# Kernel tuning notes

Measured on AMD Instinct MI355X. Metric: run time of the kernel, lower is better.

The kernel has to match this reference:

```python
import jax, jax.numpy as jnp
import numpy as np


def _forward(x, target, c0, Wm0, bm0, Wm1, bm1, Wf10, bf10, Wf11, bf11,
             Wf20, bf20, Wf21, bf21, Wh0, bh0, Wh1, bh1):
    dt = x.dtype
    F = jnp.array([[1., 0., 1., 0.], [0., 1., 0., 1.], [0., 0., 1., 0.], [0., 0., 0., 1.]], dtype=dt)
    Hm = jnp.array([[1., 0., 0., 0.], [0., 1., 0., 0.]], dtype=dt)
    G = jnp.array([[0.5, 0.], [0., 0.5], [1., 0.], [0., 1.]], dtype=dt)
    Q = 0.01 * jnp.eye(4, dtype=dt)
    R = jnp.eye(2, dtype=dt)
    B = x.shape[0]
    s0 = target[:, 0, :]                                   # [B,4] init state from label
    P0 = jnp.broadcast_to(jnp.eye(4, dtype=dt), (B, 4, 4))

    def step(carry, meas):                                  # meas: [B,2]
        c, s, P = carry                                     # [B,h],[B,4],[B,4,4]
        sn = s / 60.0
        # MUG: memory update gate
        cu = jnp.tanh(jnp.concatenate([c, sn], -1) @ Wm0 + bm0)
        cs = jnp.concatenate([cu, sn], -1)
        # SPG: state prediction gate
        d = jnp.tanh(cs @ Wf10 + bf10) @ Wf11 + bf11        # [B,2]
        s_pred = s @ F.T + d @ G.T                          # [B,4]
        pv = jnp.tanh(cs @ Wf20 + bf20) @ Wf21 + bf21       # [B,4]
        P_pred = jnp.einsum('ij,bjk,lk->bil', F, P, F) + pv[:, :, None] * pv[:, None, :] + Q
        # SUG: state update gate
        inna = meas - s_pred @ Hm.T                         # [B,2]
        hv = jnp.tanh(jnp.concatenate([cu, sn, meas / 60.0], -1) @ Wh0 + bh0) @ Wh1 + bh1
        S = jnp.einsum('ij,bjk,lk->bil', Hm, P_pred, Hm) + hv[:, :, None] * hv[:, None, :] + R
        PHt = jnp.einsum('bij,kj->bik', P_pred, Hm)         # [B,4,2]
        K = PHt @ jnp.linalg.inv(S)                         # [B,4,2]
        s_upd = s_pred + jnp.einsum('bij,bj->bi', K, inna)
        P_upd = P_pred - K @ S @ jnp.swapaxes(K, 1, 2)
        c_new = jnp.tanh(jnp.concatenate([cu, meas / 60.0, s_upd / 60.0], -1) @ Wm1 + bm1)
        return (c_new, s_upd, P_upd), s_upd

    _, outs = jax.lax.scan(step, (c0, s0, P0), jnp.swapaxes(x, 0, 1))
    return jnp.swapaxes(outs, 0, 1)                         # [B,T,4]


def setup_inputs() -> dict:
    key = jax.random.key(0)
    B, T, H, SD, MD = 2048, 128, 256, 4, 2
    ks = jax.random.split(key, 12)

    def lin(k, fin, fout):
        kw, kb = jax.random.split(k)
        sc = 1.0 / np.sqrt(fin)
        return (jax.random.uniform(kw, (fin, fout), jnp.float32, -sc, sc),
                jax.random.uniform(kb, (fout,), jnp.float32, -sc, sc))

    Wm0, bm0 = lin(ks[0], SD + H, H)
    Wm1, bm1 = lin(ks[1], SD + H + MD, H)
    Wf10, bf10 = lin(ks[2], SD + H, H)
    Wf11, bf11 = lin(ks[3], H, 2)
    Wf20, bf20 = lin(ks[4], SD + H, H)
    Wf21, bf21 = lin(ks[5], H, SD)
    Wh0, bh0 = lin(ks[6], SD + H + MD, H)
    Wh1, bh1 = lin(ks[7], H, MD)
    x = jax.random.normal(ks[8], (B, T, MD), jnp.float32) * 60.0
    target = jax.random.normal(ks[9], (B, T, SD), jnp.float32) * 60.0
    c0 = jax.random.uniform(ks[10], (B, H), jnp.float32, -0.1, 0.1)
    return dict(x=x, target=target, c0=c0, Wm0=Wm0, bm0=bm0, Wm1=Wm1, bm1=bm1,
                Wf10=Wf10, bf10=bf10, Wf11=Wf11, bf11=bf11, Wf20=Wf20, bf20=bf20,
                Wf21=Wf21, bf21=bf21, Wh0=Wh0, bh0=bh0, Wh1=Wh1, bh1=bh1)


def reference(x, target, c0, Wm0, bm0, Wm1, bm1, Wf10, bf10, Wf11, bf11,
              Wf20, bf20, Wf21, bf21, Wh0, bh0, Wh1, bh1):
    return _forward(x, target, c0, Wm0, bm0, Wm1, bm1, Wf10, bf10, Wf11, bf11,
                    Wf20, bf20, Wf21, bf21, Wh0, bh0, Wh1, bh1)
```

## Files before the change

kernel.cpp:

```cpp
#include <hip/hip_runtime.h>

typedef unsigned short u16;
typedef unsigned char  u8;
typedef signed char    s8;
typedef __bf16 bf16x8 __attribute__((ext_vector_type(8)));
typedef int    i32x4  __attribute__((ext_vector_type(4)));

#define T_STEPS 128
#define S2STR   776


__device__ __forceinline__ float bf2f(u16 h) {
  union { unsigned int u; float f; } v; v.u = ((unsigned int)h) << 16; return v.f;
}
__device__ __forceinline__ u16 f2bf(float f) {
  union { float f; unsigned int u; } v; v.f = f;
  unsigned int u = v.u;
  return (u16)((u + 0x7fffu + ((u >> 16) & 1u)) >> 16);
}
__device__ __forceinline__ unsigned int pack2(float a, float b) {
  return (unsigned int)f2bf(a) | ((unsigned int)f2bf(b) << 16);
}
__device__ __forceinline__ float clampf(float x, float lo, float hi) {
  return fmaxf(lo, fminf(x, hi));
}
__device__ __forceinline__ float tanh_fast(float x) {
  float e = __expf(2.0f * x);
  return 1.0f - 2.0f * __builtin_amdgcn_rcpf(e + 1.0f);
}
__device__ __forceinline__ int q8(float v, float s) {
  int q = __float2int_rn(v * s);
  return max(-127, min(127, q));
}
__device__ __forceinline__ unsigned int pack4q(float a, float b, float c, float d, float s) {
  return (unsigned int)(q8(a,s) & 255) | ((unsigned int)(q8(b,s) & 255) << 8) |
         ((unsigned int)(q8(c,s) & 255) << 16) | ((unsigned int)(q8(d,s) & 255) << 24);
}
__device__ __forceinline__ s8 qw(float w) {
  int q = __float2int_rn(w * 2032.0f);
  return (s8)max(-127, min(127, q));
}

__device__ __forceinline__ i32x4 mfma_i8(i32x4 a, i32x4 b, i32x4 acc) {
  asm volatile("v_mfma_i32_16x16x64_i8 %0, %1, %2, %0" : "+v"(acc) : "v"(a), "v"(b));
  return acc;
}
__device__ __forceinline__ i32x4 accfence(i32x4 acc) {
  asm volatile("s_nop 7\n\ts_nop 7" : "+v"(acc));
  return acc;
}

__global__ void egbrnn_prep(
    const float* __restrict__ Wm0, const float* __restrict__ Wm1,
    const float* __restrict__ Wf10, const float* __restrict__ Wf11,
    const float* __restrict__ Wf20, const float* __restrict__ Wf21,
    const float* __restrict__ Wh0, const float* __restrict__ Wh1,
    const float* __restrict__ bm0, const float* __restrict__ bm1,
    const float* __restrict__ bf10, const float* __restrict__ bf11,
    const float* __restrict__ bf20, const float* __restrict__ bf21,
    const float* __restrict__ bh0, const float* __restrict__ bh1,
    u8* __restrict__ ws)
{
  int idx = blockIdx.x * 256 + threadIdx.x;
  if (idx < 81920) {
    int tile = idx >> 10, r = idx & 1023;
    int lane = r >> 4, j = r & 15;
    int ft = tile / 5, kt = tile % 5;
    int m = (ft << 4) + (lane & 15);
    int k = kt * 64 + ((lane >> 4) << 4) + j;
    float w = (k < 260) ? Wm0[k * 256 + m] : 0.f;
    ((s8*)ws)[idx] = qw(w);
    return;
  }
  idx -= 81920;
  if (idx < 245760) {
    int tile = idx >> 10, r = idx & 1023;
    int lane = r >> 4, j = r & 15;
    int ft = tile / 5, kt = tile % 5;
    int F = (ft << 4) + (lane & 15);
    int k = kt * 64 + ((lane >> 4) << 4) + j;
    int sel = F >> 8, col = F & 255;
    float w = 0.f;
    if (sel == 0)      { if (k < 260) w = Wf10[k * 256 + col]; }
    else if (sel == 1) { if (k < 260) w = Wf20[k * 256 + col]; }
    else               { if (k < 262) w = Wh0 [k * 256 + col]; }
    ((s8*)ws)[81920 + idx] = qw(w);
    return;
  }
  idx -= 245760;
  if (idx < 81920) {
    int tile = idx >> 10, r = idx & 1023;
    int lane = r >> 4, j = r & 15;
    int ft = tile / 5, kt = tile % 5;
    int m = (ft << 4) + (lane & 15);
    int row = -1;
    if (kt < 4) row = kt * 64 + ((lane >> 4) << 4) + j;
    else {
      int kk = ((lane >> 4) << 4) + j;
      if (kk < 2) row = 256 + kk;
      else if (kk < 6) row = 258 + (kk - 2);
    }
    float w = (row >= 0) ? Wm1[row * 256 + m] : 0.f;
    ((s8*)ws)[327680 + idx] = qw(w);
    return;
  }
  idx -= 81920;
  if (idx < 1288) {
    float* BIAS = (float*)(ws + 409600);
    float h;
    if (idx < 256) h = bm0[idx];
    else if (idx < 1024) {
      int f = idx - 256;
      h = (f < 256) ? bf10[f] : (f < 512 ? bf20[f - 256] : bh0[f - 512]);
    } else if (idx < 1280) h = bm1[idx - 1024];
    else {
      int i2 = idx - 1280;
      h = (i2 < 2) ? bf11[i2] : (i2 < 6 ? bf21[i2 - 2] : bh1[i2 - 6]);
    }
    BIAS[idx] = h;
    return;
  }
  idx -= 1288;
  if (idx < 2048) {
    int o = idx >> 8, k = idx & 255;
    float v;
    if (o < 2)      v = Wf11[k * 2 + o];
    else if (o < 6) v = Wf21[k * 4 + (o - 2)];
    else            v = Wh1[k * 2 + (o - 6)];
    ((u16*)(ws + 414752))[idx] = f2bf(v);
  }
}

__global__ __launch_bounds__(1024, 4) void egbrnn_main(
    const float* __restrict__ x, const float* __restrict__ target,
    const float* __restrict__ c0, const u8* __restrict__ wsp,
    float* __restrict__ out)
{
  __shared__ __align__(16) u8  ACT1[5 * 1024];
  __shared__ __align__(16) u8  ACT2[6 * 1024];
  __shared__ __align__(16) u16 S2O[16 * S2STR];
  __shared__ __align__(16) u16 HWs[2048];
  __shared__ __align__(16) float SM[128];

  const float* BIAS = (const float*)(wsp + 409600);
  const float* B1 = BIAS;
  const float* B2 = BIAS + 256;
  const float* B3 = BIAS + 1024;
  const float* BS = BIAS + 1280;

  const float SA = 0.0625f / 16129.0f;
  const float SB = 0.5f / 16129.0f;
  const float SC_SN = 127.0f / 480.0f;

  const int tid = threadIdx.x;
  const int wave = tid >> 6;
  const int lane = tid & 63;
  const int nidx = lane & 15;
  const int q = lane >> 4;
  const int boff = (q << 8) + (nidx << 4);
  const int loff = lane << 4;
  const int b0 = blockIdx.x << 4;

  const int wvu = __builtin_amdgcn_readfirstlane(wave);
  const u8* pk1w  = wsp + wvu * 5120;
  const u8* pk2w0 = wsp + 81920 + wvu * 5120;
  const u8* pk2w1 = wsp + 81920 + (wvu + 16) * 5120;
  const u8* pk2w2 = wsp + 81920 + (wvu + 32) * 5120;
  const u8* pk3w  = wsp + 327680 + wvu * 5120;

  for (int i = tid; i < 2048; i += 1024) HWs[i] = ((const u16*)(wsp + 414752))[i];

  {
    int p = tid << 2;
    int tile = p >> 10, r = p & 1023;
    int b = (r >> 4) & 15;
    int kg = tile * 64 + ((r >> 8) << 4) + (r & 15);
    float4 cv = *(const float4*)(c0 + (((size_t)(b0 + b)) << 8) + kg);
    *(unsigned int*)(ACT1 + p) = pack4q(cv.x, cv.y, cv.z, cv.w, 127.0f);
  }

  float s0v = 0.f, s1v = 0.f, s2v = 0.f, s3v = 0.f;
  float P[16];
#pragma unroll
  for (int i = 0; i < 16; ++i) P[i] = 0.f;
  if (tid < 16) {
    float4 tg = *(const float4*)(target + (((size_t)(b0 + tid)) << 9));
    s0v = tg.x; s1v = tg.y; s2v = tg.z; s3v = tg.w;
    P[0] = P[5] = P[10] = P[15] = 1.f;
    unsigned int snp = pack4q(s0v, s1v, s2v, s3v, SC_SN);
    *(unsigned int*)(ACT1 + 4096 + (tid << 4)) = snp;
    *(unsigned int*)(ACT2 + 4096 + (tid << 4)) = snp;
  }
  __syncthreads();

  const int hpair = tid >> 2, hpart = tid & 3;
  const int hb = hpair & 15, ho = hpair >> 4;
  const int hcolBase = (ho < 2) ? 0 : ((ho < 6) ? 256 : 512);

  const i32x4 zero4 = {0, 0, 0, 0};

  for (int t = 0; t < T_STEPS; ++t) {
    if (tid < 16) {
      float2 mm = *(const float2*)(x + (((size_t)(b0 + tid)) << 8) + (t << 1));
      int qm0 = q8(mm.x, SC_SN), qm1 = q8(mm.y, SC_SN);
      *(u16*)(ACT2 + 4096 + (tid << 4) + 4) = (u16)((qm0 & 255) | ((qm1 & 255) << 8));
    }
    {
      i32x4 aA = zero4, aB = zero4;
#pragma unroll
      for (int kt = 0; kt < 4; ++kt) {
        i32x4 bfr = *(const i32x4*)(ACT1 + (kt << 10) + boff);
        i32x4 af  = *(const i32x4*)(pk1w + (kt << 10) + loff);
        aA = mfma_i8(af, bfr, aA);
      }
      {
        i32x4 bfr = *(const i32x4*)(ACT1 + 4096 + boff);
        i32x4 af  = *(const i32x4*)(pk1w + 4096 + loff);
        aB = mfma_i8(af, bfr, aB);
      }
      aA = accfence(aA); aB = accfence(aB);
      const int f0 = (wave << 4) + (q << 2);
      const float4 bs = *(const float4*)(B1 + f0);
      float v0 = tanh_fast(clampf((float)aA[0] * SA + (float)aB[0] * SB + bs.x, -30.f, 30.f));
      float v1 = tanh_fast(clampf((float)aA[1] * SA + (float)aB[1] * SB + bs.y, -30.f, 30.f));
      float v2 = tanh_fast(clampf((float)aA[2] * SA + (float)aB[2] * SB + bs.z, -30.f, 30.f));
      float v3 = tanh_fast(clampf((float)aA[3] * SA + (float)aB[3] * SB + bs.w, -30.f, 30.f));
      const int kk = f0 & 63;
      *(unsigned int*)(ACT2 + ((f0 >> 6) << 10) + (((f0 >> 4) & 3) << 8) + (nidx << 4) + (kk & 15)) =
          pack4q(v0, v1, v2, v3, 127.0f);
    }
    __syncthreads();
    {
      i32x4 cA[3], cB[3];
#pragma unroll
      for (int i = 0; i < 3; ++i) { cA[i] = zero4; cB[i] = zero4; }
#pragma unroll
      for (int kt = 0; kt < 5; ++kt) {
        i32x4 bfr = *(const i32x4*)(ACT2 + (kt << 10) + boff);
        i32x4 af0 = *(const i32x4*)(pk2w0 + (kt << 10) + loff);
        i32x4 af1 = *(const i32x4*)(pk2w1 + (kt << 10) + loff);
        i32x4 af2 = *(const i32x4*)(pk2w2 + (kt << 10) + loff);
        if (kt < 4) {
          cA[0] = mfma_i8(af0, bfr, cA[0]);
          cA[1] = mfma_i8(af1, bfr, cA[1]);
          cA[2] = mfma_i8(af2, bfr, cA[2]);
        } else {
          cB[0] = mfma_i8(af0, bfr, cB[0]);
          cB[1] = mfma_i8(af1, bfr, cB[1]);
          cB[2] = mfma_i8(af2, bfr, cB[2]);
        }
      }
#pragma unroll
      for (int i = 0; i < 3; ++i) {
        cA[i] = accfence(cA[i]); cB[i] = accfence(cB[i]);
        const int ft = wave + 16 * i;
        const int f0 = (ft << 4) + (q << 2);
        const float4 bs = *(const float4*)(B2 + f0);
        float v0 = tanh_fast(clampf((float)cA[i][0] * SA + (float)cB[i][0] * SB + bs.x, -30.f, 30.f));
        float v1 = tanh_fast(clampf((float)cA[i][1] * SA + (float)cB[i][1] * SB + bs.y, -30.f, 30.f));
        float v2 = tanh_fast(clampf((float)cA[i][2] * SA + (float)cB[i][2] * SB + bs.z, -30.f, 30.f));
        float v3 = tanh_fast(clampf((float)cA[i][3] * SA + (float)cB[i][3] * SB + bs.w, -30.f, 30.f));
        uint2 pv; pv.x = pack2(v0, v1); pv.y = pack2(v2, v3);
        *(uint2*)(S2O + nidx * S2STR + f0) = pv;
      }
    }
    __syncthreads();
    if (tid < 512) {
      const u16* ap = S2O + hb * S2STR + hcolBase + (hpart << 6);
      const u16* wp = HWs + (ho << 8) + (hpart << 6);
      float p = 0.f;
#pragma unroll
      for (int i = 0; i < 8; ++i) {
        bf16x8 av = *(const bf16x8*)(ap + (i << 3));
        bf16x8 wv = *(const bf16x8*)(wp + (i << 3));
#pragma unroll
        for (int j = 0; j < 8; ++j) p += (float)av[j] * (float)wv[j];
      }
      p += __shfl_xor(p, 1);
      p += __shfl_xor(p, 2);
      if (hpart == 0) SM[hb * 8 + ho] = clampf(p + BS[ho], -64.f, 64.f);
    }
    __syncthreads();
    if (tid < 16) {
      const float* sm = SM + tid * 8;
      float d0 = sm[0], d1 = sm[1];
      float pv[4] = { sm[2], sm[3], sm[4], sm[5] };
      float hv0 = sm[6], hv1 = sm[7];
      float2 mm = *(const float2*)(x + (((size_t)(b0 + tid)) << 8) + (t << 1));
      float m0 = mm.x, m1 = mm.y;
      float sp[4];
      sp[0] = s0v + s2v + 0.5f * d0;
      sp[1] = s1v + s3v + 0.5f * d1;
      sp[2] = s2v + d0;
      sp[3] = s3v + d1;
      float FP[16], Pp[16];
#pragma unroll
      for (int j = 0; j < 4; ++j) {
        FP[0 * 4 + j] = P[0 * 4 + j] + P[2 * 4 + j];
        FP[1 * 4 + j] = P[1 * 4 + j] + P[3 * 4 + j];
        FP[2 * 4 + j] = P[2 * 4 + j];
        FP[3 * 4 + j] = P[3 * 4 + j];
      }
#pragma unroll
      for (int i = 0; i < 4; ++i) {
        Pp[i * 4 + 0] = FP[i * 4 + 0] + FP[i * 4 + 2];
        Pp[i * 4 + 1] = FP[i * 4 + 1] + FP[i * 4 + 3];
        Pp[i * 4 + 2] = FP[i * 4 + 2];
        Pp[i * 4 + 3] = FP[i * 4 + 3];
      }
#pragma unroll
      for (int i = 0; i < 4; ++i)
#pragma unroll
        for (int j = 0; j < 4; ++j) Pp[i * 4 + j] += pv[i] * pv[j];
#pragma unroll
      for (int i = 0; i < 4; ++i) Pp[i * 4 + i] += 0.01f;
      float in0 = m0 - sp[0], in1 = m1 - sp[1];
      float S00 = Pp[0] + hv0 * hv0 + 1.0f;
      float S01 = Pp[1] + hv0 * hv1;
      float S10 = Pp[4] + hv1 * hv0;
      float S11 = Pp[5] + hv1 * hv1 + 1.0f;
      float det = S00 * S11 - S01 * S10;
      if (!(fabsf(det) > 1e-8f)) det = 1e-8f;
      float idet = 1.0f / det;
      float i00 =  S11 * idet, i01 = -S01 * idet, i10 = -S10 * idet, i11 = S00 * idet;
      float K[8], KS[8], su[4];
#pragma unroll
      for (int i = 0; i < 4; ++i) {
        K[i * 2 + 0] = Pp[i * 4 + 0] * i00 + Pp[i * 4 + 1] * i10;
        K[i * 2 + 1] = Pp[i * 4 + 0] * i01 + Pp[i * 4 + 1] * i11;
      }
#pragma unroll
      for (int i = 0; i < 4; ++i)
        su[i] = clampf(sp[i] + K[i * 2 + 0] * in0 + K[i * 2 + 1] * in1, -131072.f, 131072.f);
#pragma unroll
      for (int i = 0; i < 4; ++i) {
        KS[i * 2 + 0] = K[i * 2 + 0] * S00 + K[i * 2 + 1] * S10;
        KS[i * 2 + 1] = K[i * 2 + 0] * S01 + K[i * 2 + 1] * S11;
      }
#pragma unroll
      for (int i = 0; i < 4; ++i)
#pragma unroll
        for (int j = 0; j < 4; ++j)
          P[i * 4 + j] = clampf(
              Pp[i * 4 + j] - (KS[i * 2 + 0] * K[j * 2 + 0] + KS[i * 2 + 1] * K[j * 2 + 1]),
              -131072.f, 131072.f);
      s0v = su[0]; s1v = su[1]; s2v = su[2]; s3v = su[3];
      float4 ov; ov.x = su[0]; ov.y = su[1]; ov.z = su[2]; ov.w = su[3];
      *(float4*)(out + (((size_t)(b0 + tid)) << 9) + (t << 2)) = ov;
      unsigned int snp = pack4q(su[0], su[1], su[2], su[3], SC_SN);
      *(unsigned int*)(ACT1 + 4096 + (tid << 4)) = snp;
      *(unsigned int*)(ACT2 + 4096 + (tid << 4)) = snp;
      int qm0 = q8(m0, SC_SN), qm1 = q8(m1, SC_SN);
      *(unsigned int*)(ACT2 + 5120 + (tid << 4)) =
          (unsigned int)(qm0 & 255) | ((unsigned int)(qm1 & 255) << 8) |
          ((snp & 255) << 16) | (((snp >> 8) & 255) << 24);
      *(u16*)(ACT2 + 5120 + (tid << 4) + 4) = (u16)((snp >> 16) & 0xffffu);
    }
    __syncthreads();
    {
      i32x4 aA = zero4, aB = zero4;
#pragma unroll
      for (int kt = 0; kt < 4; ++kt) {
        i32x4 bfr = *(const i32x4*)(ACT2 + (kt << 10) + boff);
        i32x4 af  = *(const i32x4*)(pk3w + (kt << 10) + loff);
        aA = mfma_i8(af, bfr, aA);
      }
      {
        i32x4 bfr = *(const i32x4*)(ACT2 + 5120 + boff);
        i32x4 af  = *(const i32x4*)(pk3w + 4096 + loff);
        aB = mfma_i8(af, bfr, aB);
      }
      aA = accfence(aA); aB = accfence(aB);
      const int f0 = (wave << 4) + (q << 2);
      const float4 bs = *(const float4*)(B3 + f0);
      float v0 = tanh_fast(clampf((float)aA[0] * SA + (float)aB[0] * SB + bs.x, -30.f, 30.f));
      float v1 = tanh_fast(clampf((float)aA[1] * SA + (float)aB[1] * SB + bs.y, -30.f, 30.f));
      float v2 = tanh_fast(clampf((float)aA[2] * SA + (float)aB[2] * SB + bs.z, -30.f, 30.f));
      float v3 = tanh_fast(clampf((float)aA[3] * SA + (float)aB[3] * SB + bs.w, -30.f, 30.f));
      const int kk = f0 & 63;
      *(unsigned int*)(ACT1 + ((f0 >> 6) << 10) + (((f0 >> 4) & 3) << 8) + (nidx << 4) + (kk & 15)) =
          pack4q(v0, v1, v2, v3, 127.0f);
    }
    __syncthreads();
  }
}

extern "C" void kernel_launch(void* const* d_in, const int* in_sizes, int n_in,
                              void* d_out, int out_size, void* d_ws, size_t ws_size,
                              hipStream_t stream) {
  const float* x    = (const float*)d_in[0];
  const float* tgt  = (const float*)d_in[1];
  const float* c0   = (const float*)d_in[2];
  const float* Wm0  = (const float*)d_in[3];
  const float* bm0  = (const float*)d_in[4];
  const float* Wm1  = (const float*)d_in[5];
  const float* bm1  = (const float*)d_in[6];
  const float* Wf10 = (const float*)d_in[7];
  const float* bf10 = (const float*)d_in[8];
  const float* Wf11 = (const float*)d_in[9];
  const float* bf11 = (const float*)d_in[10];
  const float* Wf20 = (const float*)d_in[11];
  const float* bf20 = (const float*)d_in[12];
  const float* Wf21 = (const float*)d_in[13];
  const float* bf21 = (const float*)d_in[14];
  const float* Wh0  = (const float*)d_in[15];
  const float* bh0  = (const float*)d_in[16];
  const float* Wh1  = (const float*)d_in[17];
  const float* bh1  = (const float*)d_in[18];
  u8* ws     = (u8*)d_ws;
  float* out = (float*)d_out;

  egbrnn_prep<<<dim3(1614), dim3(256), 0, stream>>>(
      Wm0, Wm1, Wf10, Wf11, Wf20, Wf21, Wh0, Wh1,
      bm0, bm1, bf10, bf11, bf20, bf21, bh0, bh1, ws);
  egbrnn_main<<<dim3(128), dim3(1024), 0, stream>>>(x, tgt, c0, ws, out);
}
```

Before: 928.8 us.

## Stage first gate weights in LDS and pad head-stage smem rows to avoid bank conflicts

The packed int8 weights for the first memory-update GEMM (80 KB) are copied into shared memory once per block, so each timestep reads them from LDS rather than global/L2. The bf16 S2O activations and head weights are re-laid out with a 16-byte pad every 64 elements to reduce LDS bank conflicts in the small head dot products. The extra 80 KB of LDS per block can lower occupancy (the launch bounds ask for 4 blocks) and adds a one-time copy cost.

```diff
diff --git a/kernel.cpp b/kernel.cpp
--- a/kernel.cpp
+++ b/kernel.cpp
@@ -7,7 +7,8 @@
 typedef int    i32x4  __attribute__((ext_vector_type(4)));
 
 #define T_STEPS 128
-#define S2STR   776
+#define S2ROW 1744
+#define HWROW 560
 
 
 __device__ __forceinline__ float bf2f(u16 h) {
@@ -136,10 +137,11 @@
     const float* __restrict__ c0, const u8* __restrict__ wsp,
     float* __restrict__ out)
 {
-  __shared__ __align__(16) u8  ACT1[5 * 1024];
-  __shared__ __align__(16) u8  ACT2[6 * 1024];
-  __shared__ __align__(16) u16 S2O[16 * S2STR];
-  __shared__ __align__(16) u16 HWs[2048];
+  __shared__ __align__(16) u8 LPK1[81920];
+  __shared__ __align__(16) u8 ACT1[5 * 1024];
+  __shared__ __align__(16) u8 ACT2[6 * 1024];
+  __shared__ __align__(16) u8 S2O[16 * S2ROW];
+  __shared__ __align__(16) u8 HWs[8 * HWROW];
   __shared__ __align__(16) float SM[128];
 
   const float* BIAS = (const float*)(wsp + 409600);
@@ -162,13 +164,19 @@
   const int b0 = blockIdx.x << 4;
 
   const int wvu = __builtin_amdgcn_readfirstlane(wave);
-  const u8* pk1w  = wsp + wvu * 5120;
   const u8* pk2w0 = wsp + 81920 + wvu * 5120;
   const u8* pk2w1 = wsp + 81920 + (wvu + 16) * 5120;
   const u8* pk2w2 = wsp + 81920 + (wvu + 32) * 5120;
   const u8* pk3w  = wsp + 327680 + wvu * 5120;
-
-  for (int i = tid; i < 2048; i += 1024) HWs[i] = ((const u16*)(wsp + 414752))[i];
+  const u8* lpk1w = LPK1 + wvu * 5120;
+
+  for (int i = tid; i < 5120; i += 1024)
+    *(i32x4*)(LPK1 + (i << 4)) = *(const i32x4*)(wsp + (i << 4));
+
+  for (int i = tid; i < 2048; i += 1024) {
+    int o = i >> 8, k = i & 255;
+    *(u16*)(HWs + o * HWROW + (k << 1) + ((k >> 6) << 4)) = ((const u16*)(wsp + 414752))[i];
+  }
 
   {
     int p = tid << 2;
@@ -196,6 +204,9 @@
   const int hpair = tid >> 2, hpart = tid & 3;
   const int hb = hpair & 15, ho = hpair >> 4;
   const int hcolBase = (ho < 2) ? 0 : ((ho < 6) ? 256 : 512);
+  const int hf = hcolBase + (hpart << 6);
+  const int hapOff = hb * S2ROW + (hf << 1) + ((hf >> 6) << 4);
+  const int hwpOff = ho * HWROW + hpart * 144;
 
   const i32x4 zero4 = {0, 0, 0, 0};
 
@@ -210,12 +221,12 @@
 #pragma unroll
       for (int kt = 0; kt < 4; ++kt) {
         i32x4 bfr = *(const i32x4*)(ACT1 + (kt << 10) + boff);
-        i32x4 af  = *(const i32x4*)(pk1w + (kt << 10) + loff);
+        i32x4 af  = *(const i32x4*)(lpk1w + (kt << 10) + loff);
         aA = mfma_i8(af, bfr, aA);
       }
       {
         i32x4 bfr = *(const i32x4*)(ACT1 + 4096 + boff);
-        i32x4 af  = *(const i32x4*)(pk1w + 4096 + loff);
+        i32x4 af  = *(const i32x4*)(lpk1w + 4096 + loff);
         aB = mfma_i8(af, bfr, aB);
       }
       aA = accfence(aA); aB = accfence(aB);
@@ -225,8 +236,7 @@
       float v1 = tanh_fast(clampf((float)aA[1] * SA + (float)aB[1] * SB + bs.y, -30.f, 30.f));
       float v2 = tanh_fast(clampf((float)aA[2] * SA + (float)aB[2] * SB + bs.z, -30.f, 30.f));
       float v3 = tanh_fast(clampf((float)aA[3] * SA + (float)aB[3] * SB + bs.w, -30.f, 30.f));
-      const int kk = f0 & 63;
-      *(unsigned int*)(ACT2 + ((f0 >> 6) << 10) + (((f0 >> 4) & 3) << 8) + (nidx << 4) + (kk & 15)) =
+      *(unsigned int*)(ACT2 + ((f0 >> 6) << 10) + (((f0 >> 4) & 3) << 8) + (nidx << 4) + (f0 & 15)) =
           pack4q(v0, v1, v2, v3, 127.0f);
     }
     __syncthreads();
@@ -261,18 +271,18 @@
         float v2 = tanh_fast(clampf((float)cA[i][2] * SA + (float)cB[i][2] * SB + bs.z, -30.f, 30.f));
         float v3 = tanh_fast(clampf((float)cA[i][3] * SA + (float)cB[i][3] * SB + bs.w, -30.f, 30.f));
         uint2 pv; pv.x = pack2(v0, v1); pv.y = pack2(v2, v3);
-        *(uint2*)(S2O + nidx * S2STR + f0) = pv;
+        *(uint2*)(S2O + nidx * S2ROW + (f0 << 1) + ((f0 >> 6) << 4)) = pv;
       }
     }
     __syncthreads();
     if (tid < 512) {
-      const u16* ap = S2O + hb * S2STR + hcolBase + (hpart << 6);
-      const u16* wp = HWs + (ho << 8) + (hpart << 6);
+      const u8* ap = S2O + hapOff;
+      const u8* wp = HWs + hwpOff;
       float p = 0.f;
 #pragma unroll
       for (int i = 0; i < 8; ++i) {
-        bf16x8 av = *(const bf16x8*)(ap + (i << 3));
-        bf16x8 wv = *(const bf16x8*)(wp + (i << 3));
+        bf16x8 av = *(const bf16x8*)(ap + (i << 4));
+        bf16x8 wv = *(const bf16x8*)(wp + (i << 4));
 #pragma unroll
         for (int j = 0; j < 8; ++j) p += (float)av[j] * (float)wv[j];
       }
@@ -377,8 +387,7 @@
       float v1 = tanh_fast(clampf((float)aA[1] * SA + (float)aB[1] * SB + bs.y, -30.f, 30.f));
       float v2 = tanh_fast(clampf((float)aA[2] * SA + (float)aB[2] * SB + bs.z, -30.f, 30.f));
       float v3 = tanh_fast(clampf((float)aA[3] * SA + (float)aB[3] * SB + bs.w, -30.f, 30.f));
-      const int kk = f0 & 63;
-      *(unsigned int*)(ACT1 + ((f0 >> 6) << 10) + (((f0 >> 4) & 3) << 8) + (nidx << 4) + (kk & 15)) =
+      *(unsigned int*)(ACT1 + ((f0 >> 6) << 10) + (((f0 >> 4) & 3) << 8) + (nidx << 4) + (f0 & 15)) =
           pack4q(v0, v1, v2, v3, 127.0f);
     }
     __syncthreads();
```

Measured after the change: 899.5 us. 3.2% less time.
